# Kernel tuning notes

Hardware: AMD Instinct MI355X
Metric: run time of the kernel (lower is better)

## Reference

```python
import jax, jax.numpy as jnp
import numpy as np

EPS = 1e-5

def _bn(x, w, b, rm, rv):
    # eval-mode BatchNorm over channel axis (x: [..., C] broadcastable)
    return (x - rm) * (w * jax.lax.rsqrt(rv + EPS)) + b

def setup_inputs() -> dict:
    key = jax.random.key(0)
    ks = jax.random.split(key, 20)
    B, C, H, W = 2, 64, 96, 96
    Cq = C // 8  # query/key channels
    Cr = C // 8  # SE reduction channels
    s = 0.05
    inp = {
        'x': jax.random.normal(ks[0], (B, C, H, W), jnp.float32),
        'wq': jax.random.normal(ks[1], (Cq, C), jnp.float32) * s,
        'bq': jnp.zeros((Cq,), jnp.float32),
        'wk': jax.random.normal(ks[2], (Cq, C), jnp.float32) * s,
        'bk': jnp.zeros((Cq,), jnp.float32),
        'wv': jax.random.normal(ks[3], (C, C), jnp.float32) * s,
        'bv': jnp.zeros((C,), jnp.float32),
        'gamma': jnp.full((1,), 0.5, jnp.float32),
        'bn_w': jnp.ones((C,), jnp.float32),
        'bn_b': jnp.zeros((C,), jnp.float32),
        'bn_rm': jax.random.normal(ks[4], (C,), jnp.float32) * 0.1,
        'bn_rv': jax.random.uniform(ks[5], (C,), jnp.float32) + 0.5,
        'se_w1': jax.random.normal(ks[6], (Cr, C), jnp.float32) * s,
        'se_b1': jnp.zeros((Cr,), jnp.float32),
        'se_bn1_w': jnp.ones((Cr,), jnp.float32),
        'se_bn1_b': jnp.zeros((Cr,), jnp.float32),
        'se_bn1_rm': jax.random.normal(ks[7], (Cr,), jnp.float32) * 0.1,
        'se_bn1_rv': jax.random.uniform(ks[8], (Cr,), jnp.float32) + 0.5,
        'se_w2': jax.random.normal(ks[9], (C, Cr), jnp.float32) * s,
        'se_b2': jnp.zeros((C,), jnp.float32),
        'se_bn2_w': jnp.ones((C,), jnp.float32),
        'se_bn2_b': jnp.zeros((C,), jnp.float32),
        'se_bn2_rm': jax.random.normal(ks[10], (C,), jnp.float32) * 0.1,
        'se_bn2_rv': jax.random.uniform(ks[11], (C,), jnp.float32) + 0.5,
    }
    return inp

def reference(x, wq, bq, wk, bk, wv, bv, gamma, bn_w, bn_b, bn_rm, bn_rv,
              se_w1, se_b1, se_bn1_w, se_bn1_b, se_bn1_rm, se_bn1_rv,
              se_w2, se_b2, se_bn2_w, se_bn2_b, se_bn2_rm, se_bn2_rv):
    B, C, H, W = x.shape
    N = H * W
    xf = x.reshape(B, C, N)
    # PAM branch: 1x1 conv projections
    q = jnp.einsum('oc,bcn->bno', wq, xf) + bq            # [B,N,C/8]
    k = jnp.einsum('oc,bcn->bon', wk, xf) + bk[:, None]    # [B,C/8,N]
    v = jnp.einsum('oc,bcn->bon', wv, xf) + bv[:, None]    # [B,C,N]
    energy = jnp.einsum('bno,bom->bnm', q, k)              # [B,N,N]
    attn = jax.nn.softmax(energy, axis=-1)
    # out[b,c,i] = sum_j v[b,c,j] * attn[b,i,j]  (bmm(V, attn^T))
    out = jnp.einsum('bcj,bij->bci', v, attn)
    out = gamma[0] * out
    out = _bn(out, bn_w[:, None], bn_b[:, None], bn_rm[:, None], bn_rv[:, None])
    pam = out.reshape(B, C, H, W)
    # SE branch: GAP + 1x1 conv-bn-relu x2, multiplicative gate
    a = xf.mean(axis=2)                                    # [B,C]
    a1 = jax.nn.relu(_bn(a @ se_w1.T + se_b1, se_bn1_w, se_bn1_b, se_bn1_rm, se_bn1_rv))
    a2 = jax.nn.relu(_bn(a1 @ se_w2.T + se_b2, se_bn2_w, se_bn2_b, se_bn2_rm, se_bn2_rv))
    se = x * a2[:, :, None, None]
    return x + se + pam
```

## Files before the change

### kernel.cpp

```cpp
#include <hip/hip_runtime.h>
#include <hip/hip_bf16.h>

#define B_SZ   2
#define C_CH   64
#define NQ     8
#define QKS    16
#define NPIX   9216
#define NKS    576
#define QBLKS  288
#define KPART  4
#define NSPLIT 4
#define KEYS_W 576
#define NCHUNK_W 9
#define SM_F   2080
#define PSLOT  2080
#define NP4    2304
#define KSTEP2 1024
#define VSTEP  4096

typedef short bf16x8 __attribute__((ext_vector_type(8)));
typedef float f32x4  __attribute__((ext_vector_type(4)));
typedef float f32x16 __attribute__((ext_vector_type(16)));
typedef unsigned u32x4 __attribute__((ext_vector_type(4)));
typedef unsigned uint2v __attribute__((ext_vector_type(2)));

static __device__ __forceinline__ unsigned pack2bf(float a, float b){
    unsigned r;
    asm("v_cvt_pk_bf16_f32 %0, %1, %2" : "=v"(r) : "v"(a), "v"(b));
    return r;
}

static __device__ __forceinline__ float exp2r(float x){
    return __builtin_amdgcn_exp2f(x);
}

__global__ __launch_bounds__(256) void prep_kernel(
    const float* __restrict__ x,
    const float* __restrict__ wq, const float* __restrict__ bq,
    const float* __restrict__ wk, const float* __restrict__ bk,
    const float* __restrict__ wv, const float* __restrict__ bv,
    __hip_bfloat16* __restrict__ qp, __hip_bfloat16* __restrict__ kp,
    __hip_bfloat16* __restrict__ vswz, float* __restrict__ amean)
{
    const int blk = blockIdx.x, tid = threadIdx.x;
    if (blk < 144){
        int t  = blk*256 + tid;
        int n  = (t % NP4) * 4;
        int c8 = (t / NP4) & 7;
        int b  = t / (NP4*8);
        c8 = __builtin_amdgcn_readfirstlane(c8);
        b  = __builtin_amdgcn_readfirstlane(b);
        float acc[8][4];
#pragma unroll
        for (int k = 0; k < 8; ++k){
            float bvv = bv[c8*8 + k];
            acc[k][0] = bvv; acc[k][1] = bvv; acc[k][2] = bvv; acc[k][3] = bvv;
        }
#pragma unroll 4
        for (int ci = 0; ci < C_CH; ++ci){
            const float4 xv = *reinterpret_cast<const float4*>(
                x + (size_t)(b*C_CH + ci)*NPIX + n);
#pragma unroll
            for (int k = 0; k < 8; ++k){
                float w = wv[(c8*8 + k)*C_CH + ci];
                acc[k][0] = fmaf(xv.x, w, acc[k][0]);
                acc[k][1] = fmaf(xv.y, w, acc[k][1]);
                acc[k][2] = fmaf(xv.z, w, acc[k][2]);
                acc[k][3] = fmaf(xv.w, w, acc[k][3]);
            }
        }
#pragma unroll
        for (int k = 0; k < 8; ++k){
            int c = c8*8 + k;
            size_t base = ((size_t)((b*NKS + (n >> 4))*2 + (c >> 5)))*512
                        + (((n >> 3) & 1) << 8) + ((c & 31) << 3) + (n & 7);
            unsigned long long wpk =
                (unsigned long long)pack2bf(acc[k][0], acc[k][1]) |
                ((unsigned long long)pack2bf(acc[k][2], acc[k][3]) << 32);
            *reinterpret_cast<unsigned long long*>(vswz + base) = wpk;
        }
    } else if (blk < 180){
        int t  = (blk - 144)*256 + tid;
        int n  = (t % NP4) * 4;
        int o8 = (t / NP4) & 1;
        int b  = t / (NP4*2);
        o8 = __builtin_amdgcn_readfirstlane(o8);
        b  = __builtin_amdgcn_readfirstlane(b);
        const bool isq = (o8 == 0);
        const float* w    = isq ? wq : wk;
        const float* bias = isq ? bq : bk;
        float acc[8][4];
#pragma unroll
        for (int k = 0; k < 8; ++k){
            float bb = bias[k];
            acc[k][0] = bb; acc[k][1] = bb; acc[k][2] = bb; acc[k][3] = bb;
        }
#pragma unroll 4
        for (int ci = 0; ci < C_CH; ++ci){
            const float4 xv = *reinterpret_cast<const float4*>(
                x + (size_t)(b*C_CH + ci)*NPIX + n);
#pragma unroll
            for (int k = 0; k < 8; ++k){
                float wv_ = w[k*C_CH + ci];
                acc[k][0] = fmaf(xv.x, wv_, acc[k][0]);
                acc[k][1] = fmaf(xv.y, wv_, acc[k][1]);
                acc[k][2] = fmaf(xv.z, wv_, acc[k][2]);
                acc[k][3] = fmaf(xv.w, wv_, acc[k][3]);
            }
        }
        if (isq){
#pragma unroll
            for (int k = 0; k < 8; ++k)
#pragma unroll
                for (int px = 0; px < 4; ++px) acc[k][px] *= 1.44269504f;
        }
        __hip_bfloat16* dst = isq ? qp : kp;
        u32x4 zr; zr[0] = 0; zr[1] = 0; zr[2] = 0; zr[3] = 0;
#pragma unroll
        for (int px = 0; px < 4; ++px){
            u32x4 row;
            row[0] = pack2bf(acc[0][px], acc[1][px]);
            row[1] = pack2bf(acc[2][px], acc[3][px]);
            row[2] = pack2bf(acc[4][px], acc[5][px]);
            row[3] = pack2bf(acc[6][px], acc[7][px]);
            __hip_bfloat16* d0 = dst + ((size_t)(b*NPIX + n + px))*QKS;
            *reinterpret_cast<u32x4*>(d0)     = row;
            *reinterpret_cast<u32x4*>(d0 + 8) = zr;
        }
    } else {
        int bc = blk - 180;
        float s = 0.f;
        for (int i = tid; i < NPIX; i += 256) s += x[(size_t)bc*NPIX + i];
#pragma unroll
        for (int o = 32; o > 0; o >>= 1) s += __shfl_down(s, o, 64);
        __shared__ float red[4];
        if ((tid & 63) == 0) red[tid >> 6] = s;
        __syncthreads();
        if (tid == 0) amean[bc] = (red[0] + red[1] + red[2] + red[3]) * (1.f / (float)NPIX);
    }
}

__global__ __launch_bounds__(256) void flash_fused(
    const __hip_bfloat16* __restrict__ qp,
    const __hip_bfloat16* __restrict__ kp,
    const __hip_bfloat16* __restrict__ vswz,
    float* __restrict__ pws)
{
    __shared__ __align__(16) float sm[2*SM_F];

    const int qt2 = blockIdx.x, b = blockIdx.y, z = blockIdx.z;
    const int p  = threadIdx.x >> 6;
    const int l  = threadIdx.x & 63;
    const int lc = l & 31;
    const int lh = l >> 5;

    bf16x8 qfrag = *reinterpret_cast<const bf16x8*>(
        qp + ((size_t)(b*NPIX + qt2*32 + lc))*QKS + lh*8);

    bf16x8 ones;
#pragma unroll
    for (int i = 0; i < 8; ++i) ones[i] = (short)0x3F80;

    f32x16 zero16;
#pragma unroll
    for (int i = 0; i < 16; ++i) zero16[i] = 0.f;

    f32x16 Of0 = zero16, Of1 = zero16;
    f32x16 Lacc = zero16;

    const int kpart = z*KPART + p;
    const __hip_bfloat16* kptr = kp + ((size_t)(b*NPIX + kpart*KEYS_W + lc))*QKS + lh*8;
    const __hip_bfloat16* vptr = vswz + ((size_t)((b*NKS + kpart*(KEYS_W/16))*2))*512 + l*8;

    auto CHUNK = [&](const bf16x8& k0, const bf16x8& k1){
        bf16x8 vf[8];
#pragma unroll
        for (int t = 0; t < 8; ++t)
            vf[t] = *reinterpret_cast<const bf16x8*>(vptr + t*512);
        vptr += VSTEP;

        unsigned D[16];
#pragma unroll
        for (int kt = 0; kt < 2; ++kt){
            f32x16 s = __builtin_amdgcn_mfma_f32_32x32x16_bf16(
                kt ? k1 : k0, qfrag, zero16, 0, 0, 0);
#pragma unroll
            for (int g = 0; g < 4; ++g){
                float e0 = exp2r(s[4*g+0]), e1 = exp2r(s[4*g+1]);
                float e2 = exp2r(s[4*g+2]), e3 = exp2r(s[4*g+3]);
                D[kt*8 + g*2 + 0] = pack2bf(e0, e1);
                D[kt*8 + g*2 + 1] = pack2bf(e2, e3);
            }
        }
        __builtin_amdgcn_s_setprio(1);
#pragma unroll
        for (int ks = 0; ks < 4; ++ks){
            const int base = (ks >> 1)*8 + (ks & 1)*4;
            uint2v r0 = __builtin_amdgcn_permlane32_swap(D[base+0], D[base+2], false, false);
            uint2v r1 = __builtin_amdgcn_permlane32_swap(D[base+1], D[base+3], false, false);
            u32x4 pu; pu[0] = r0[0]; pu[1] = r1[0]; pu[2] = r0[1]; pu[3] = r1[1];
            bf16x8 pf = __builtin_bit_cast(bf16x8, pu);
            Of0  = __builtin_amdgcn_mfma_f32_32x32x16_bf16(vf[ks*2+0], pf, Of0, 0, 0, 0);
            Of1  = __builtin_amdgcn_mfma_f32_32x32x16_bf16(vf[ks*2+1], pf, Of1, 0, 0, 0);
            Lacc = __builtin_amdgcn_mfma_f32_32x32x16_bf16(ones,       pf, Lacc, 0, 0, 0);
        }
        __builtin_amdgcn_s_setprio(0);
    };

    bf16x8 kA0, kA1, kB0, kB1;
    kA0 = *reinterpret_cast<const bf16x8*>(kptr);
    kA1 = *reinterpret_cast<const bf16x8*>(kptr + 512);
    kptr += KSTEP2;
    for (int it = 0; it < 4; ++it){
        kB0 = *reinterpret_cast<const bf16x8*>(kptr);
        kB1 = *reinterpret_cast<const bf16x8*>(kptr + 512);
        kptr += KSTEP2;
        CHUNK(kA0, kA1);
        if (it < 3){
            kA0 = *reinterpret_cast<const bf16x8*>(kptr);
            kA1 = *reinterpret_cast<const bf16x8*>(kptr + 512);
            kptr += KSTEP2;
        } else {
            kA0 = *reinterpret_cast<const bf16x8*>(kptr);
            kA1 = *reinterpret_cast<const bf16x8*>(kptr + 512);
        }
        CHUNK(kB0, kB1);
    }
    CHUNK(kA0, kA1);

    if (p >= 2){
        const int ps = p - 2;
#pragma unroll
        for (int r = 0; r < 16; ++r){
            sm[ps*SM_F +        r*64 + l] = Of0[r];
            sm[ps*SM_F + 1024 + r*64 + l] = Of1[r];
        }
        if (l < 32) sm[ps*SM_F + 2048 + l] = Lacc[0];
    }
    __syncthreads();
    if (p < 2){
#pragma unroll
        for (int r = 0; r < 16; ++r){
            sm[p*SM_F +        r*64 + l] += Of0[r];
            sm[p*SM_F + 1024 + r*64 + l] += Of1[r];
        }
        if (l < 32) sm[p*SM_F + 2048 + l] += Lacc[0];
    }
    __syncthreads();

    {
        float* dst = pws + ((size_t)((b*QBLKS + qt2)*NSPLIT + z))*PSLOT;
        for (int i = threadIdx.x; i < PSLOT; i += 256)
            dst[i] = sm[i] + sm[SM_F + i];
    }
}

__global__ __launch_bounds__(256) void combine_kernel(
    const float* __restrict__ pws,
    const float* __restrict__ amean,
    const float* __restrict__ sw1, const float* __restrict__ sb1,
    const float* __restrict__ s1w, const float* __restrict__ s1b,
    const float* __restrict__ s1m, const float* __restrict__ s1v,
    const float* __restrict__ sw2, const float* __restrict__ sb2,
    const float* __restrict__ s2w, const float* __restrict__ s2b,
    const float* __restrict__ s2m, const float* __restrict__ s2v,
    const float* __restrict__ x,
    const float* __restrict__ gamma,
    const float* __restrict__ bnw, const float* __restrict__ bnb,
    const float* __restrict__ bnm, const float* __restrict__ bnv,
    float* __restrict__ out)
{
    const int qt2 = blockIdx.x, b = blockIdx.y;
    const int p  = threadIdx.x >> 6;
    const int l  = threadIdx.x & 63;
    const int lc = l & 31;
    const int lh = l >> 5;

    float a1r;
    {
        int r8 = l & 7;
        float s = sb1[r8];
#pragma unroll 8
        for (int c = 0; c < C_CH; ++c)
            s = fmaf(amean[b*C_CH + c], sw1[r8*C_CH + c], s);
        s = (s - s1m[r8]) * (s1w[r8] * rsqrtf(s1v[r8] + 1e-5f)) + s1b[r8];
        a1r = fmaxf(s, 0.f);
    }

    const float* P0 = pws + ((size_t)((b*QBLKS + qt2)*NSPLIT))*PSLOT;

    const int i   = lc;
    const int cgs = p*2 + lh;
    float gam = gamma[0];

    float a1g[8];
#pragma unroll
    for (int j = 0; j < 8; ++j) a1g[j] = __shfl(a1r, (l & 56) | j, 64);

    float L = 0.f;
#pragma unroll
    for (int zz = 0; zz < NSPLIT; ++zz) L += P0[zz*PSLOT + 2048 + i];
    float invL = 1.f / L;
    int n = qt2*32 + i;
#pragma unroll
    for (int r = 0; r < 8; ++r){
        int c = cgs*8 + r;
        float s = sb2[c];
#pragma unroll
        for (int j = 0; j < 8; ++j) s = fmaf(a1g[j], sw2[c*NQ + j], s);
        s = (s - s2m[c]) * (s2w[c] * rsqrtf(s2v[c] + 1e-5f)) + s2b[c];
        float a2v = fmaxf(s, 0.f);

        int c5   = c & 31;
        int reg  = (c5 & 3) + 4*(c5 >> 3);
        int lsrc = (c5 >> 2) & 1;
        int o    = (c >> 5)*1024 + reg*64 + lsrc*32 + i;
        float O = 0.f;
#pragma unroll
        for (int zz = 0; zz < NSPLIT; ++zz) O += P0[zz*PSLOT + o];
        float pam = gam * O * invL;
        pam = (pam - bnm[c]) * (bnw[c] * rsqrtf(bnv[c] + 1e-5f)) + bnb[c];
        float xv = x[(size_t)(b*C_CH + c)*NPIX + n];
        out[(size_t)(b*C_CH + c)*NPIX + n] = fmaf(xv, a2v, xv + pam);
    }
}

extern "C" void kernel_launch(void* const* d_in, const int* in_sizes, int n_in,
                              void* d_out, int out_size, void* d_ws, size_t ws_size,
                              hipStream_t stream)
{
    const float* x     = (const float*)d_in[0];
    const float* wq    = (const float*)d_in[1];
    const float* bq    = (const float*)d_in[2];
    const float* wk    = (const float*)d_in[3];
    const float* bk    = (const float*)d_in[4];
    const float* wv    = (const float*)d_in[5];
    const float* bv    = (const float*)d_in[6];
    const float* gamma = (const float*)d_in[7];
    const float* bnw   = (const float*)d_in[8];
    const float* bnb   = (const float*)d_in[9];
    const float* bnm   = (const float*)d_in[10];
    const float* bnv   = (const float*)d_in[11];
    const float* sw1   = (const float*)d_in[12];
    const float* sb1   = (const float*)d_in[13];
    const float* s1w   = (const float*)d_in[14];
    const float* s1b   = (const float*)d_in[15];
    const float* s1m   = (const float*)d_in[16];
    const float* s1v   = (const float*)d_in[17];
    const float* sw2   = (const float*)d_in[18];
    const float* sb2   = (const float*)d_in[19];
    const float* s2w   = (const float*)d_in[20];
    const float* s2b   = (const float*)d_in[21];
    const float* s2m   = (const float*)d_in[22];
    const float* s2v   = (const float*)d_in[23];

    size_t off = 0;
    auto give = [&](size_t bytes) -> void* {
        void* r = (char*)d_ws + off;
        off += (bytes + 255) & ~(size_t)255;
        return r;
    };
    __hip_bfloat16* qp   = (__hip_bfloat16*)give((size_t)B_SZ*NPIX*QKS*2);
    __hip_bfloat16* kp   = (__hip_bfloat16*)give((size_t)B_SZ*NPIX*QKS*2);
    __hip_bfloat16* vswz = (__hip_bfloat16*)give((size_t)B_SZ*C_CH*NPIX*2);
    float* amean = (float*)give((size_t)B_SZ*C_CH*4);
    float* pws   = (float*)give((size_t)B_SZ*QBLKS*NSPLIT*PSLOT*4);

    prep_kernel<<<dim3(308), dim3(256), 0, stream>>>(x, wq, bq, wk, bk, wv, bv,
                                                     qp, kp, vswz, amean);
    flash_fused<<<dim3(QBLKS, B_SZ, NSPLIT), dim3(256), 0, stream>>>(qp, kp, vswz, pws);
    combine_kernel<<<dim3(QBLKS, B_SZ), dim3(256), 0, stream>>>(
        pws, amean,
        sw1, sb1, s1w, s1b, s1m, s1v,
        sw2, sb2, s2w, s2b, s2m, s2v,
        x, gamma, bnw, bnb, bnm, bnv, (float*)d_out);
}
```

Before: 171.5 us.

## Fuse combine into flash kernel via last-block atomic counter

Merges the split-K combine/epilogue kernel into the flash attention kernel. Each block writes its partial result, fences, and bumps a per-query-tile atomic counter; the last of the NSPLIT blocks performs the combine, SE gate and output write. Counters are zeroed in prep_kernel. This removes one kernel launch and the gap between kernels, and lets the combine overlap with other blocks' attention work, at the cost of atomics, fences and a tail of serialized combines.

New measurement: 425.6 us. +148.2%, slower.

```diff
diff --git a/kernel.cpp b/kernel.cpp
--- a/kernel.cpp
+++ b/kernel.cpp
@@ -11,12 +11,12 @@
 #define KPART  4
 #define NSPLIT 4
 #define KEYS_W 576
-#define NCHUNK_W 9
 #define SM_F   2080
 #define PSLOT  2080
 #define NP4    2304
 #define KSTEP2 1024
 #define VSTEP  4096
+#define NCTR   (B_SZ*QBLKS)
 
 typedef short bf16x8 __attribute__((ext_vector_type(8)));
 typedef float f32x4  __attribute__((ext_vector_type(4)));
@@ -40,7 +40,8 @@
     const float* __restrict__ wk, const float* __restrict__ bk,
     const float* __restrict__ wv, const float* __restrict__ bv,
     __hip_bfloat16* __restrict__ qp, __hip_bfloat16* __restrict__ kp,
-    __hip_bfloat16* __restrict__ vswz, float* __restrict__ amean)
+    __hip_bfloat16* __restrict__ vswz, float* __restrict__ amean,
+    int* __restrict__ ctr)
 {
     const int blk = blockIdx.x, tid = threadIdx.x;
     if (blk < 144){
@@ -129,6 +130,8 @@
         }
     } else {
         int bc = blk - 180;
+        if (bc == 0)
+            for (int i = tid; i < NCTR; i += 256) ctr[i] = 0;
         float s = 0.f;
         for (int i = tid; i < NPIX; i += 256) s += x[(size_t)bc*NPIX + i];
 #pragma unroll
@@ -144,119 +147,7 @@
     const __hip_bfloat16* __restrict__ qp,
     const __hip_bfloat16* __restrict__ kp,
     const __hip_bfloat16* __restrict__ vswz,
-    float* __restrict__ pws)
-{
-    __shared__ __align__(16) float sm[2*SM_F];
-
-    const int qt2 = blockIdx.x, b = blockIdx.y, z = blockIdx.z;
-    const int p  = threadIdx.x >> 6;
-    const int l  = threadIdx.x & 63;
-    const int lc = l & 31;
-    const int lh = l >> 5;
-
-    bf16x8 qfrag = *reinterpret_cast<const bf16x8*>(
-        qp + ((size_t)(b*NPIX + qt2*32 + lc))*QKS + lh*8);
-
-    bf16x8 ones;
-#pragma unroll
-    for (int i = 0; i < 8; ++i) ones[i] = (short)0x3F80;
-
-    f32x16 zero16;
-#pragma unroll
-    for (int i = 0; i < 16; ++i) zero16[i] = 0.f;
-
-    f32x16 Of0 = zero16, Of1 = zero16;
-    f32x16 Lacc = zero16;
-
-    const int kpart = z*KPART + p;
-    const __hip_bfloat16* kptr = kp + ((size_t)(b*NPIX + kpart*KEYS_W + lc))*QKS + lh*8;
-    const __hip_bfloat16* vptr = vswz + ((size_t)((b*NKS + kpart*(KEYS_W/16))*2))*512 + l*8;
-
-    auto CHUNK = [&](const bf16x8& k0, const bf16x8& k1){
-        bf16x8 vf[8];
-#pragma unroll
-        for (int t = 0; t < 8; ++t)
-            vf[t] = *reinterpret_cast<const bf16x8*>(vptr + t*512);
-        vptr += VSTEP;
-
-        unsigned D[16];
-#pragma unroll
-        for (int kt = 0; kt < 2; ++kt){
-            f32x16 s = __builtin_amdgcn_mfma_f32_32x32x16_bf16(
-                kt ? k1 : k0, qfrag, zero16, 0, 0, 0);
-#pragma unroll
-            for (int g = 0; g < 4; ++g){
-                float e0 = exp2r(s[4*g+0]), e1 = exp2r(s[4*g+1]);
-                float e2 = exp2r(s[4*g+2]), e3 = exp2r(s[4*g+3]);
-                D[kt*8 + g*2 + 0] = pack2bf(e0, e1);
-                D[kt*8 + g*2 + 1] = pack2bf(e2, e3);
-            }
-        }
-        __builtin_amdgcn_s_setprio(1);
-#pragma unroll
-        for (int ks = 0; ks < 4; ++ks){
-            const int base = (ks >> 1)*8 + (ks & 1)*4;
-            uint2v r0 = __builtin_amdgcn_permlane32_swap(D[base+0], D[base+2], false, false);
-            uint2v r1 = __builtin_amdgcn_permlane32_swap(D[base+1], D[base+3], false, false);
-            u32x4 pu; pu[0] = r0[0]; pu[1] = r1[0]; pu[2] = r0[1]; pu[3] = r1[1];
-            bf16x8 pf = __builtin_bit_cast(bf16x8, pu);
-            Of0  = __builtin_amdgcn_mfma_f32_32x32x16_bf16(vf[ks*2+0], pf, Of0, 0, 0, 0);
-            Of1  = __builtin_amdgcn_mfma_f32_32x32x16_bf16(vf[ks*2+1], pf, Of1, 0, 0, 0);
-            Lacc = __builtin_amdgcn_mfma_f32_32x32x16_bf16(ones,       pf, Lacc, 0, 0, 0);
-        }
-        __builtin_amdgcn_s_setprio(0);
-    };
-
-    bf16x8 kA0, kA1, kB0, kB1;
-    kA0 = *reinterpret_cast<const bf16x8*>(kptr);
-    kA1 = *reinterpret_cast<const bf16x8*>(kptr + 512);
-    kptr += KSTEP2;
-    for (int it = 0; it < 4; ++it){
-        kB0 = *reinterpret_cast<const bf16x8*>(kptr);
-        kB1 = *reinterpret_cast<const bf16x8*>(kptr + 512);
-        kptr += KSTEP2;
-        CHUNK(kA0, kA1);
-        if (it < 3){
-            kA0 = *reinterpret_cast<const bf16x8*>(kptr);
-            kA1 = *reinterpret_cast<const bf16x8*>(kptr + 512);
-            kptr += KSTEP2;
-        } else {
-            kA0 = *reinterpret_cast<const bf16x8*>(kptr);
-            kA1 = *reinterpret_cast<const bf16x8*>(kptr + 512);
-        }
-        CHUNK(kB0, kB1);
-    }
-    CHUNK(kA0, kA1);
-
-    if (p >= 2){
-        const int ps = p - 2;
-#pragma unroll
-        for (int r = 0; r < 16; ++r){
-            sm[ps*SM_F +        r*64 + l] = Of0[r];
-            sm[ps*SM_F + 1024 + r*64 + l] = Of1[r];
-        }
-        if (l < 32) sm[ps*SM_F + 2048 + l] = Lacc[0];
-    }
-    __syncthreads();
-    if (p < 2){
-#pragma unroll
-        for (int r = 0; r < 16; ++r){
-            sm[p*SM_F +        r*64 + l] += Of0[r];
-            sm[p*SM_F + 1024 + r*64 + l] += Of1[r];
-        }
-        if (l < 32) sm[p*SM_F + 2048 + l] += Lacc[0];
-    }
-    __syncthreads();
-
-    {
-        float* dst = pws + ((size_t)((b*QBLKS + qt2)*NSPLIT + z))*PSLOT;
-        for (int i = threadIdx.x; i < PSLOT; i += 256)
-            dst[i] = sm[i] + sm[SM_F + i];
-    }
-}
-
-__global__ __launch_bounds__(256) void combine_kernel(
-    const float* __restrict__ pws,
+    float* __restrict__ pws, int* __restrict__ ctr,
     const float* __restrict__ amean,
     const float* __restrict__ sw1, const float* __restrict__ sb1,
     const float* __restrict__ s1w, const float* __restrict__ s1b,
@@ -270,11 +161,116 @@
     const float* __restrict__ bnm, const float* __restrict__ bnv,
     float* __restrict__ out)
 {
-    const int qt2 = blockIdx.x, b = blockIdx.y;
+    __shared__ __align__(16) float sm[2*SM_F];
+
+    const int qt2 = blockIdx.x, b = blockIdx.y, z = blockIdx.z;
     const int p  = threadIdx.x >> 6;
     const int l  = threadIdx.x & 63;
     const int lc = l & 31;
     const int lh = l >> 5;
+
+    bf16x8 qfrag = *reinterpret_cast<const bf16x8*>(
+        qp + ((size_t)(b*NPIX + qt2*32 + lc))*QKS + lh*8);
+
+    bf16x8 ones;
+#pragma unroll
+    for (int i = 0; i < 8; ++i) ones[i] = (short)0x3F80;
+
+    f32x16 zero16;
+#pragma unroll
+    for (int i = 0; i < 16; ++i) zero16[i] = 0.f;
+
+    f32x16 Of0 = zero16, Of1 = zero16;
+    f32x16 Lacc = zero16;
+
+    const int kpart = z*KPART + p;
+    const __hip_bfloat16* kptr = kp + ((size_t)(b*NPIX + kpart*KEYS_W + lc))*QKS + lh*8;
+    const __hip_bfloat16* vptr = vswz + ((size_t)((b*NKS + kpart*(KEYS_W/16))*2))*512 + l*8;
+
+    auto CHUNK = [&](const bf16x8& k0, const bf16x8& k1){
+        bf16x8 vf[8];
+#pragma unroll
+        for (int t = 0; t < 8; ++t)
+            vf[t] = *reinterpret_cast<const bf16x8*>(vptr + t*512);
+        vptr += VSTEP;
+
+        unsigned D[16];
+#pragma unroll
+        for (int kt = 0; kt < 2; ++kt){
+            f32x16 s = __builtin_amdgcn_mfma_f32_32x32x16_bf16(
+                kt ? k1 : k0, qfrag, zero16, 0, 0, 0);
+#pragma unroll
+            for (int g = 0; g < 4; ++g){
+                float e0 = exp2r(s[4*g+0]), e1 = exp2r(s[4*g+1]);
+                float e2 = exp2r(s[4*g+2]), e3 = exp2r(s[4*g+3]);
+                D[kt*8 + g*2 + 0] = pack2bf(e0, e1);
+                D[kt*8 + g*2 + 1] = pack2bf(e2, e3);
+            }
+        }
+        __builtin_amdgcn_s_setprio(1);
+#pragma unroll
+        for (int ks = 0; ks < 4; ++ks){
+            const int base = (ks >> 1)*8 + (ks & 1)*4;
+            uint2v r0 = __builtin_amdgcn_permlane32_swap(D[base+0], D[base+2], false, false);
+            uint2v r1 = __builtin_amdgcn_permlane32_swap(D[base+1], D[base+3], false, false);
+            u32x4 pu; pu[0] = r0[0]; pu[1] = r1[0]; pu[2] = r0[1]; pu[3] = r1[1];
+            bf16x8 pf = __builtin_bit_cast(bf16x8, pu);
+            Of0  = __builtin_amdgcn_mfma_f32_32x32x16_bf16(vf[ks*2+0], pf, Of0, 0, 0, 0);
+            Of1  = __builtin_amdgcn_mfma_f32_32x32x16_bf16(vf[ks*2+1], pf, Of1, 0, 0, 0);
+            Lacc = __builtin_amdgcn_mfma_f32_32x32x16_bf16(ones,       pf, Lacc, 0, 0, 0);
+        }
+        __builtin_amdgcn_s_setprio(0);
+    };
+
+    bf16x8 kA0, kA1, kB0, kB1;
+    kA0 = *reinterpret_cast<const bf16x8*>(kptr);
+    kA1 = *reinterpret_cast<const bf16x8*>(kptr + 512);
+    kptr += KSTEP2;
+    for (int it = 0; it < 4; ++it){
+        kB0 = *reinterpret_cast<const bf16x8*>(kptr);
+        kB1 = *reinterpret_cast<const bf16x8*>(kptr + 512);
+        kptr += KSTEP2;
+        CHUNK(kA0, kA1);
+        kA0 = *reinterpret_cast<const bf16x8*>(kptr);
+        kA1 = *reinterpret_cast<const bf16x8*>(kptr + 512);
+        if (it < 3) kptr += KSTEP2;
+        CHUNK(kB0, kB1);
+    }
+    CHUNK(kA0, kA1);
+
+    if (p >= 2){
+        const int ps = p - 2;
+#pragma unroll
+        for (int r = 0; r < 16; ++r){
+            sm[ps*SM_F +        r*64 + l] = Of0[r];
+            sm[ps*SM_F + 1024 + r*64 + l] = Of1[r];
+        }
+        if (l < 32) sm[ps*SM_F + 2048 + l] = Lacc[0];
+    }
+    __syncthreads();
+    if (p < 2){
+#pragma unroll
+        for (int r = 0; r < 16; ++r){
+            sm[p*SM_F +        r*64 + l] += Of0[r];
+            sm[p*SM_F + 1024 + r*64 + l] += Of1[r];
+        }
+        if (l < 32) sm[p*SM_F + 2048 + l] += Lacc[0];
+    }
+    __syncthreads();
+
+    {
+        float* dst = pws + ((size_t)((b*QBLKS + qt2)*NSPLIT + z))*PSLOT;
+        for (int i = threadIdx.x; i < PSLOT; i += 256)
+            dst[i] = sm[i] + sm[SM_F + i];
+    }
+
+    __threadfence();
+    __shared__ int lastFlag;
+    if (threadIdx.x == 0)
+        lastFlag = (atomicAdd(&ctr[b*QBLKS + qt2], 1) == NSPLIT - 1);
+    __syncthreads();
+    if (!lastFlag) return;
+    __threadfence();
 
     float a1r;
     {
@@ -288,7 +284,6 @@
     }
 
     const float* P0 = pws + ((size_t)((b*QBLKS + qt2)*NSPLIT))*PSLOT;
-
     const int i   = lc;
     const int cgs = p*2 + lh;
     float gam = gamma[0];
@@ -365,12 +360,12 @@
     __hip_bfloat16* vswz = (__hip_bfloat16*)give((size_t)B_SZ*C_CH*NPIX*2);
     float* amean = (float*)give((size_t)B_SZ*C_CH*4);
     float* pws   = (float*)give((size_t)B_SZ*QBLKS*NSPLIT*PSLOT*4);
+    int*   ctr   = (int*)give((size_t)NCTR*4);
 
     prep_kernel<<<dim3(308), dim3(256), 0, stream>>>(x, wq, bq, wk, bk, wv, bv,
-                                                     qp, kp, vswz, amean);
-    flash_fused<<<dim3(QBLKS, B_SZ, NSPLIT), dim3(256), 0, stream>>>(qp, kp, vswz, pws);
-    combine_kernel<<<dim3(QBLKS, B_SZ), dim3(256), 0, stream>>>(
-        pws, amean,
+                                                     qp, kp, vswz, amean, ctr);
+    flash_fused<<<dim3(QBLKS, B_SZ, NSPLIT), dim3(256), 0, stream>>>(
+        qp, kp, vswz, pws, ctr, amean,
         sw1, sb1, s1w, s1b, s1m, s1v,
         sw2, sb2, s2w, s2b, s2m, s2v,
         x, gamma, bnw, bnb, bnm, bnv, (float*)d_out);
```
